# Performance work log

Hardware: AMD Instinct MI355X
Metric: run time of the kernel (lower is better)

## Reference

```python
import jax, jax.numpy as jnp
import numpy as np

GROUP_SIZES = [2048, 4096, 8192, 16384]
TOP_K = 64
L1_COEFF = 1e-3
AUX_PENALTY = 1e-2
N_BATCHES_TO_DEAD = 20
AUX_K_MULT = 16


def setup_inputs() -> dict:
    D = 1024
    S = sum(GROUP_SIZES)  # 30720
    B = 2048
    key = jax.random.key(0)
    k1, k2, k3 = jax.random.split(key, 3)
    x = jax.random.normal(k1, (B, D), dtype=jnp.float32)
    # kaiming_uniform-like init for W_enc [D, S]
    bound = np.sqrt(6.0 / D)
    W_enc = jax.random.uniform(k2, (D, S), jnp.float32, -bound, bound)
    # W_dec = W_enc.T row-normalized (as in __init__)
    W_dec = W_enc.T
    W_dec = W_dec / jnp.linalg.norm(W_dec, axis=-1, keepdims=True)
    b_dec = jnp.zeros((D,), jnp.float32)
    b_enc = jnp.zeros((S,), jnp.float32)
    num_batches_not_active = jax.random.randint(k3, (S,), 0, 40, dtype=jnp.int32)
    return dict(x=x, b_dec=b_dec, b_enc=b_enc, W_enc=W_enc, W_dec=W_dec,
                num_batches_not_active=num_batches_not_active)


def reference(x, b_dec, b_enc, W_enc, W_dec, num_batches_not_active):
    B, D = x.shape
    S = W_enc.shape[1]
    # encoder
    acts = jax.nn.relu((x - b_dec) @ W_enc + b_enc)  # [B, S]
    # global (batch-level) top-k over flattened activations + scatter back
    k = TOP_K * B
    flat = acts.reshape(-1)
    vals, idx = jax.lax.top_k(flat, k)
    acts_topk = jnp.zeros_like(flat).at[idx].set(vals).reshape(B, S)
    # hierarchical group-wise decode with per-group L2 losses
    bounds = np.concatenate([[0], np.cumsum(GROUP_SIZES)]).astype(int)
    recon = jnp.broadcast_to(b_dec, (B, D))
    l2_losses = []
    for i in range(len(GROUP_SIZES)):
        s, e = int(bounds[i]), int(bounds[i + 1])
        recon = recon + acts_topk[:, s:e] @ W_dec[s:e, :]
        l2_losses.append(jnp.mean((recon - x) ** 2))
    mean_l2_loss = jnp.mean(jnp.stack(l2_losses))
    l1_loss = L1_COEFF * jnp.mean(jnp.sum(jnp.abs(acts_topk), axis=-1))
    # auxiliary dead-feature loss
    dead = num_batches_not_active >= N_BATCHES_TO_DEAD  # [S] bool
    residual = jax.lax.stop_gradient(x - recon)
    k_aux = TOP_K * AUX_K_MULT * B  # assumes num_dead * B >= k_aux (holds here)
    masked = jnp.where(dead[None, :], acts, -jnp.inf)
    min_top_k_val = jax.lax.top_k(masked.reshape(-1), k_aux)[0][-1]
    min_top_k_val = jnp.where(jnp.isfinite(min_top_k_val), min_top_k_val, 0.0)
    acts_aux = jax.nn.relu(acts - min_top_k_val) * dead[None, :].astype(acts.dtype)
    recon_aux = acts_aux @ W_dec  # dead-only contribution (others zeroed)
    aux_loss = AUX_PENALTY * jnp.mean((recon_aux - residual) ** 2)
    aux_loss = jnp.where(jnp.any(dead), aux_loss, 0.0)
    total_loss = mean_l2_loss + l1_loss + aux_loss
    l0_norm = jnp.mean(jnp.sum((acts_topk > 0).astype(jnp.float32), axis=-1))
    return total_loss, mean_l2_loss, l1_loss, aux_loss, l0_norm, acts_topk, recon
```

## Files before the change

kernel.cpp:

```cpp
#include <hip/hip_runtime.h>

#define NB 2048
#define ND 1024
#define NS 30720
#define K_MAIN 131072LL
#define K_AUX  2097152LL
#define BAND_CAP 16384
#define SEL_CAP  8192
#define CANDA_CAP 65536
#define EPS_BAND 1e-3f
#define KSPLIT 4

#define OFF_SCAL 0
#define OFF_ACC  256
#define OFF_H1M  512
#define OFF_H1A  16896
#define OFF_H2M  33280
#define OFF_H2A  49664
#define OFF_ZERO_END 66048
#define OFF_DEAD 66048
#define OFF_SEL_IDX 98304
#define OFF_SEL_BITS 131072
#define OFF_BANDI 163840
#define OFF_BANDV 229376
#define OFF_CAB  360448
#define OFF_RAUX 1048576ULL
#define OFF_AH   (OFF_RAUX + (unsigned long long)KSPLIT * NB * ND * 4)
#define OFF_AL   (OFF_AH + 2048ULL*1024*2)
#define OFF_WHT  (OFF_AL + 2048ULL*1024*2)
#define OFF_WLT  (OFF_WHT + 30720ULL*1024*2)
#define WS_NEED_ENC (OFF_WLT + 30720ULL*1024*2)
#define OFF_AXB  OFF_AH
#define OFF_WDT  (OFF_AXB + 2048ULL*30720*2)
#define WS_NEED_AUX (OFF_WDT + 1024ULL*30720*2)

#define S_NDEAD 0
#define S_B1M 1
#define S_REM1M 2
#define S_B1A 3
#define S_REM1A 4
#define S_T24M 5
#define S_BLO 6
#define S_BHI 7
#define S_T24A 8
#define S_JA 9
#define S_NHI 10
#define S_BANDC 11
#define S_CCA 12
#define S_SELCNT 13
#define S_L0 14
#define S_MINBITS 15

#define A_L2_0 0
#define A_L1 4
#define A_AUX 5

typedef __attribute__((ext_vector_type(8))) short bf16x8;
typedef __attribute__((ext_vector_type(4))) float f32x4;

__device__ __forceinline__ float blk_reduce(float v, float* sred) {
    int t = threadIdx.x;
    #pragma unroll
    for (int o = 32; o > 0; o >>= 1) v += __shfl_down(v, o, 64);
    __syncthreads();
    if ((t & 63) == 0) sred[t >> 6] = v;
    __syncthreads();
    return sred[0] + sred[1] + sred[2] + sred[3];
}

__device__ __forceinline__ unsigned short f2bf(float f) {
    unsigned u = __float_as_uint(f);
    unsigned r = (u + 0x7FFFu + ((u >> 16) & 1u)) >> 16;
    return (unsigned short)r;
}
__device__ __forceinline__ float bf2f(unsigned short h) {
    return __uint_as_float(((unsigned)h) << 16);
}

#define GLD16(gp, lp) __builtin_amdgcn_global_load_lds( \
    (const __attribute__((address_space(1))) unsigned int*)(gp), \
    (__attribute__((address_space(3))) unsigned int*)(lp), 16, 0, 0)

__global__ void k_init(int* w) {
    int n = OFF_ZERO_END / 4;
    for (int i = blockIdx.x * blockDim.x + threadIdx.x; i < n; i += gridDim.x * blockDim.x)
        w[i] = 0;
}

__global__ void k_dead(const int* __restrict__ nbna, unsigned char* __restrict__ dead, int* scal) {
    int stride = gridDim.x * blockDim.x;
    int cnt = 0;
    for (int i = blockIdx.x * blockDim.x + threadIdx.x; i < NS; i += stride) {
        bool d = nbna[i] >= 20;
        dead[i] = d ? 1 : 0;
        cnt += d ? 1 : 0;
    }
    #pragma unroll
    for (int o = 32; o > 0; o >>= 1) cnt += __shfl_down(cnt, o, 64);
    if ((threadIdx.x & 63) == 0 && cnt) atomicAdd(&scal[S_NDEAD], cnt);
}

__global__ void k_prep_a(const float* __restrict__ x, const float* __restrict__ b_dec,
                         unsigned short* __restrict__ Ahg, unsigned short* __restrict__ Alg) {
    int stride = gridDim.x * blockDim.x;
    for (int i = blockIdx.x * blockDim.x + threadIdx.x; i < NB * ND; i += stride) {
        float v = x[i] - b_dec[i & (ND - 1)];
        unsigned short h = f2bf(v);
        unsigned short l = f2bf(v - bf2f(h));
        Ahg[i] = h; Alg[i] = l;
    }
}

__global__ __launch_bounds__(256) void k_prep_w(const float* __restrict__ W,
        unsigned short* __restrict__ WhT, unsigned short* __restrict__ WlT) {
    __shared__ float tile[32][33];
    int n0 = blockIdx.x * 32, k0 = blockIdx.y * 32;
    int t = threadIdx.x;
    int c = t & 31, r = t >> 5;
    #pragma unroll
    for (int it = 0; it < 4; it++)
        tile[r + it * 8][c] = W[(size_t)(k0 + r + it * 8) * NS + n0 + c];
    __syncthreads();
    int kl = t & 31, nl = t >> 5;
    #pragma unroll
    for (int it = 0; it < 4; it++) {
        float v = tile[kl][nl + it * 8];
        unsigned short h = f2bf(v);
        unsigned short l = f2bf(v - bf2f(h));
        size_t o = (size_t)(n0 + nl + it * 8) * ND + k0 + kl;
        WhT[o] = h; WlT[o] = l;
    }
}

#define ENC_STAGE(bufoff, p, gptr, r, ktn) GLD16((gptr) + (size_t)(r) * 128 * ND + (size_t)(ktn) * 32, \
    smem + (bufoff) + (p) * 8192 + (r) * 4096 + ldsw)

#define ENC_RD_AH(boff) { _Pragma("unroll") \
    for (int i = 0; i < 8; i++) ah[i] = *(const bf16x8*)&smem[(boff) + (arb + i * 16) * 32 + cph8]; }
#define ENC_RD_AL(boff) { _Pragma("unroll") \
    for (int i = 0; i < 8; i++) al[i] = *(const bf16x8*)&smem[(boff) + 8192 + (arb + i * 16) * 32 + cph8]; }
#define ENC_RD_BH(boff) { _Pragma("unroll") \
    for (int j = 0; j < 4; j++) bh[j] = *(const bf16x8*)&smem[(boff) + 2 * 8192 + (brb + j * 16) * 32 + cph8]; }
#define ENC_RD_BL(boff) { _Pragma("unroll") \
    for (int j = 0; j < 4; j++) bl[j] = *(const bf16x8*)&smem[(boff) + 3 * 8192 + (brb + j * 16) * 32 + cph8]; }

#define ENC_MFMA(AF, BF) { \
    asm volatile("s_waitcnt lgkmcnt(0)" ::: "memory"); \
    __builtin_amdgcn_sched_barrier(0); \
    __builtin_amdgcn_s_setprio(1); \
    _Pragma("unroll") for (int i = 0; i < 8; i++) \
        _Pragma("unroll") for (int j = 0; j < 4; j++) \
            acc[i][j] = __builtin_amdgcn_mfma_f32_16x16x32_bf16(AF[i], BF[j], acc[i][j], 0, 0, 0); \
    __builtin_amdgcn_s_setprio(0); }

__global__ __launch_bounds__(512, 2) void k_enc_mfma(
        const unsigned short* __restrict__ Ahg, const unsigned short* __restrict__ Alg,
        const unsigned short* __restrict__ WhT, const unsigned short* __restrict__ WlT,
        const float* __restrict__ b_enc, const unsigned char* __restrict__ dead,
        float* __restrict__ acts, int* __restrict__ h1m, int* __restrict__ h1a) {
    __shared__ unsigned short smem[65536];
    const int t = threadIdx.x;
    const int lane = t & 63, w = t >> 6;
    const int wm = w >> 2, wn = w & 3;
    const int flat = blockIdx.x;
    const int wg = (flat & 7) * 120 + (flat >> 3);
    const int n0 = (wg >> 3) * 256;
    const int m0 = (wg & 7) * 256;
    const int ln15 = lane & 15, q = lane >> 4;
    const int cph8 = ((q ^ ((lane >> 1) & 3)) << 3);

    const int srow = w * 16 + (lane >> 2);
    const int sq8 = (((lane & 3) ^ ((lane >> 3) & 3)) << 3);
    const unsigned short* gA  = Ahg + (size_t)(m0 + srow) * ND + sq8;
    const unsigned short* gAl = Alg + (size_t)(m0 + srow) * ND + sq8;
    const unsigned short* gB  = WhT + (size_t)(n0 + srow) * ND + sq8;
    const unsigned short* gBl = WlT + (size_t)(n0 + srow) * ND + sq8;
    const int ldsw = w * 512;

    f32x4 acc[8][4];
    #pragma unroll
    for (int i = 0; i < 8; i++)
        #pragma unroll
        for (int j = 0; j < 4; j++) acc[i][j] = (f32x4){0.f, 0.f, 0.f, 0.f};

    const int arb = wm * 128 + ln15;
    const int brb = wn * 64 + ln15;

    ENC_STAGE(0, 0, gA, 0, 0);  ENC_STAGE(0, 0, gA, 1, 0);
    ENC_STAGE(0, 2, gB, 0, 0);  ENC_STAGE(0, 2, gB, 1, 0);
    ENC_STAGE(0, 3, gBl, 0, 0); ENC_STAGE(0, 3, gBl, 1, 0);
    ENC_STAGE(0, 1, gAl, 0, 0); ENC_STAGE(0, 1, gAl, 1, 0);

    for (int kt = 0; kt < 31; ++kt) {
        const int cboff = (kt & 1) * 32768;
        const int nboff = cboff ^ 32768;
        const int kn = kt + 1;
        bf16x8 ah[8], bh[4], bl[4], al[8];

        ENC_STAGE(nboff, 0, gA, 0, kn);  ENC_STAGE(nboff, 0, gA, 1, kn);
        ENC_STAGE(nboff, 2, gB, 0, kn);  ENC_STAGE(nboff, 2, gB, 1, kn);
        asm volatile("s_waitcnt vmcnt(8)" ::: "memory");
        __builtin_amdgcn_s_barrier();
        ENC_RD_AH(cboff) ENC_RD_BH(cboff)
        ENC_MFMA(ah, bh)

        ENC_STAGE(nboff, 3, gBl, 0, kn); ENC_STAGE(nboff, 3, gBl, 1, kn);
        ENC_STAGE(nboff, 1, gAl, 0, kn); ENC_STAGE(nboff, 1, gAl, 1, kn);
        asm volatile("s_waitcnt vmcnt(8)" ::: "memory");
        __builtin_amdgcn_s_barrier();
        ENC_RD_BL(cboff)
        ENC_MFMA(ah, bl)

        ENC_RD_AL(cboff)
        ENC_MFMA(al, bh)
    }

    {
        const int cboff = 32768;
        bf16x8 ah[8], bh[4], bl[4], al[8];
        asm volatile("s_waitcnt vmcnt(4)" ::: "memory");
        __builtin_amdgcn_s_barrier();
        ENC_RD_AH(cboff) ENC_RD_BH(cboff)
        ENC_MFMA(ah, bh)
        asm volatile("s_waitcnt vmcnt(0)" ::: "memory");
        __builtin_amdgcn_s_barrier();
        ENC_RD_BL(cboff)
        ENC_MFMA(ah, bl)
        ENC_RD_AL(cboff)
        ENC_MFMA(al, bh)
    }

    __syncthreads();
    int* hm = (int*)smem;
    int* ha = hm + 4096;
    for (int i2 = t; i2 < 8192; i2 += 512) hm[i2] = 0;
    __syncthreads();

    int zc = 0, zca = 0;
    #pragma unroll
    for (int j = 0; j < 4; j++) {
        int n = n0 + wn * 64 + j * 16 + ln15;
        float be = b_enc[n];
        bool dd = dead[n] != 0;
        #pragma unroll
        for (int i = 0; i < 8; i++) {
            int mrow = m0 + wm * 128 + i * 16 + q * 4;
            #pragma unroll
            for (int rg = 0; rg < 4; rg++) {
                float v = fmaxf(acc[i][j][rg] + be, 0.f);
                acts[(size_t)(mrow + rg) * NS + n] = v;
                unsigned bits = __float_as_uint(v);
                if (bits == 0u) { zc++; zca += dd ? 1 : 0; }
                else {
                    atomicAdd(&hm[bits >> 20], 1);
                    if (dd) atomicAdd(&ha[bits >> 20], 1);
                }
            }
        }
    }
    #pragma unroll
    for (int o = 32; o > 0; o >>= 1) { zc += __shfl_down(zc, o, 64); zca += __shfl_down(zca, o, 64); }
    if ((t & 63) == 0) { if (zc) atomicAdd(&hm[0], zc); if (zca) atomicAdd(&ha[0], zca); }
    __syncthreads();
    for (int i2 = t; i2 < 4096; i2 += 512) {
        if (hm[i2]) atomicAdd(&h1m[i2], hm[i2]);
        if (ha[i2]) atomicAdd(&h1a[i2], ha[i2]);
    }
}

#define GBM 128
#define GBN 128
#define GBK 8
__global__ __launch_bounds__(256) void k_enc_gemm(const float* __restrict__ x,
        const float* __restrict__ b_dec, const float* __restrict__ b_enc,
        const float* __restrict__ W, float* __restrict__ acts) {
    __shared__ float As[GBK][GBM];
    __shared__ float Bs[GBK][GBN];
    const int t = threadIdx.x;
    const int tx = t & 15, ty = t >> 4;
    const int m0 = blockIdx.y * GBM, n0 = blockIdx.x * GBN;
    const int am = t >> 1, ak = (t & 1) * 4;
    const int bk = t >> 5, bnq = (t & 31) * 4;
    float acc[8][8];
    #pragma unroll
    for (int i = 0; i < 8; i++)
        #pragma unroll
        for (int j = 0; j < 8; j++) acc[i][j] = 0.f;
    for (int k0 = 0; k0 < ND; k0 += GBK) {
        float4 av = *(const float4*)(x + (size_t)(m0 + am) * ND + k0 + ak);
        float4 bd = *(const float4*)(b_dec + k0 + ak);
        As[ak + 0][am] = av.x - bd.x;
        As[ak + 1][am] = av.y - bd.y;
        As[ak + 2][am] = av.z - bd.z;
        As[ak + 3][am] = av.w - bd.w;
        *(float4*)&Bs[bk][bnq] = *(const float4*)(W + (size_t)(k0 + bk) * NS + n0 + bnq);
        __syncthreads();
        #pragma unroll
        for (int kk = 0; kk < GBK; kk++) {
            float a[8], b[8];
            *(float4*)&a[0] = *(const float4*)&As[kk][ty * 4];
            *(float4*)&a[4] = *(const float4*)&As[kk][64 + ty * 4];
            *(float4*)&b[0] = *(const float4*)&Bs[kk][tx * 4];
            *(float4*)&b[4] = *(const float4*)&Bs[kk][64 + tx * 4];
            #pragma unroll
            for (int i = 0; i < 8; i++)
                #pragma unroll
                for (int j = 0; j < 8; j++)
                    acc[i][j] = fmaf(a[i], b[j], acc[i][j]);
        }
        __syncthreads();
    }
    float be[8];
    #pragma unroll
    for (int j = 0; j < 4; j++) {
        be[j]     = b_enc[n0 + tx * 4 + j];
        be[4 + j] = b_enc[n0 + 64 + tx * 4 + j];
    }
    #pragma unroll
    for (int i = 0; i < 8; i++) {
        int row = m0 + ((i < 4) ? (ty * 4 + i) : (64 + ty * 4 + i - 4));
        float* orow = acts + (size_t)row * NS + n0;
        #pragma unroll
        for (int j = 0; j < 4; j++) {
            orow[tx * 4 + j]      = fmaxf(acc[i][j] + be[j], 0.f);
            orow[64 + tx * 4 + j] = fmaxf(acc[i][4 + j] + be[4 + j], 0.f);
        }
    }
}

__global__ __launch_bounds__(256) void k_hist1(const float* __restrict__ acts,
        const unsigned char* __restrict__ dead, int* h1m, int* h1a) {
    __shared__ int hm[4096], ha[4096];
    int t = threadIdx.x;
    for (int i = t; i < 4096; i += 256) { hm[i] = 0; ha[i] = 0; }
    __syncthreads();
    for (int row = blockIdx.x; row < NB; row += gridDim.x) {
        const float* pr = acts + (size_t)row * NS;
        for (int c = t; c < NS; c += 256) {
            unsigned bits = __float_as_uint(pr[c]);
            bool isz = (bits == 0u);
            bool dd = dead[c] != 0;
            unsigned long long mz = __ballot(isz);
            unsigned long long mza = __ballot(isz && dd);
            if ((t & 63) == 0) {
                int nz = __popcll(mz);
                if (nz) atomicAdd(&hm[0], nz);
                int nza = __popcll(mza);
                if (nza) atomicAdd(&ha[0], nza);
            }
            if (!isz) {
                atomicAdd(&hm[bits >> 20], 1);
                if (dd) atomicAdd(&ha[bits >> 20], 1);
            }
        }
    }
    __syncthreads();
    for (int i = t; i < 4096; i += 256) {
        if (hm[i]) atomicAdd(&h1m[i], hm[i]);
        if (ha[i]) atomicAdd(&h1a[i], ha[i]);
    }
}

__global__ void k_scan(const int* __restrict__ hist, int* scal, int mode) {
    __shared__ long long csum[256];
    __shared__ long long totsh;
    int t = threadIdx.x;
    int base = t * 16;
    int h[16];
    long long loc = 0;
    #pragma unroll
    for (int i = 0; i < 16; i++) { h[i] = hist[base + i]; loc += h[i]; }
    csum[t] = loc;
    __syncthreads();
    if (t == 0) {
        long long run = 0;
        for (int c = 255; c >= 0; c--) { long long tmp = csum[c]; csum[c] = run; run += tmp; }
        totsh = run;
    }
    __syncthreads();
    long long k;
    if (mode == 0) k = K_MAIN;
    else if (mode == 1) k = K_AUX;
    else if (mode == 2) k = (long long)scal[S_REM1M];
    else {
        if (scal[S_B1A] < 0) { if (t == 0) { scal[S_T24A] = -1; scal[S_MINBITS] = 0; } return; }
        k = (long long)scal[S_REM1A];
    }
    if (mode == 1 && k > totsh) { if (t == 0) scal[S_B1A] = -1; return; }
    long long cum = csum[t];
    int fb = -1; long long rem = 0;
    for (int i = 15; i >= 0; i--) {
        long long ca = cum;
        cum += h[i];
        if (ca < k && k <= cum) { fb = base + i; rem = k - ca; }
    }
    if (fb >= 0) {
        if (mode == 0)      { scal[S_B1M] = fb; scal[S_REM1M] = (int)rem; }
        else if (mode == 1) { scal[S_B1A] = fb; scal[S_REM1A] = (int)rem; }
        else if (mode == 2) {
            int t24 = (scal[S_B1M] << 12) | fb;
            scal[S_T24M] = t24;
            float center = __uint_as_float((((unsigned)t24) << 8) | 128u);
            float lo = center - EPS_BAND;
            if (lo < 0.f) lo = 0.f;
            scal[S_BLO] = (int)__float_as_uint(lo);
            scal[S_BHI] = (int)__float_as_uint(center + EPS_BAND);
        }
        else { scal[S_T24A] = (scal[S_B1A] << 12) | fb; scal[S_JA] = (int)rem; }
    }
}

__global__ __launch_bounds__(256) void k_hist2(const float* __restrict__ acts,
        const unsigned char* __restrict__ dead, const int* scal, int* h2m, int* h2a) {
    int b1m = scal[S_B1M], b1a = scal[S_B1A];
    int row = blockIdx.x, t = threadIdx.x;
    const float* pr = acts + (size_t)row * NS;
    for (int c = t; c < NS; c += 256) {
        unsigned bits = __float_as_uint(pr[c]);
        int hi = (int)(bits >> 20);
        if (hi == b1m) atomicAdd(&h2m[(bits >> 8) & 0xFFF], 1);
        if (b1a >= 0 && hi == b1a && dead[c]) atomicAdd(&h2a[(bits >> 8) & 0xFFF], 1);
    }
}

__global__ __launch_bounds__(256) void k_collect(const float* __restrict__ acts,
        const unsigned char* __restrict__ dead, int* scal,
        int* bandi, unsigned* cab) {
    int row = blockIdx.x, t = threadIdx.x;
    unsigned blo = (unsigned)scal[S_BLO], bhi = (unsigned)scal[S_BHI];
    int t24a = scal[S_T24A];
    const float* pr = acts + (size_t)row * NS;
    int cnt = 0;
    for (int c = t; c < NS; c += 256) {
        unsigned bits = __float_as_uint(pr[c]);
        if (bits > bhi) cnt++;
        else if (bits >= blo) {
            int p = atomicAdd(&scal[S_BANDC], 1);
            if (p < BAND_CAP) bandi[p] = row * NS + c;
        }
        if (t24a >= 0 && (bits >> 8) == (unsigned)t24a && dead[c]) {
            int p = atomicAdd(&scal[S_CCA], 1);
            if (p < CANDA_CAP) cab[p] = bits;
        }
    }
    #pragma unroll
    for (int o = 32; o > 0; o >>= 1) cnt += __shfl_down(cnt, o, 64);
    __shared__ int s2[4];
    if ((t & 63) == 0) s2[t >> 6] = cnt;
    __syncthreads();
    if (t == 0) {
        int tot = s2[0] + s2[1] + s2[2] + s2[3];
        if (tot) atomicAdd(&scal[S_NHI], tot);
    }
}

__global__ __launch_bounds__(256) void k_resolve(const unsigned* __restrict__ cab, int* scal) {
    __shared__ int h[256];
    int t = threadIdx.x;
    h[t] = 0;
    __syncthreads();
    int t24a = scal[S_T24A];
    if (t24a < 0) { if (t == 0) scal[S_MINBITS] = 0; return; }
    int cnt = min(scal[S_CCA], CANDA_CAP);
    int ja = scal[S_JA];
    for (int e = t; e < cnt; e += 256) atomicAdd(&h[cab[e] & 0xFF], 1);
    __syncthreads();
    if (t == 0) {
        long long cum = 0; int L = 0;
        for (int b = 255; b >= 0; b--) {
            long long ca = cum; cum += h[b];
            if (ca < ja && ja <= cum) { L = b; break; }
        }
        scal[S_MINBITS] = (int)((((unsigned)t24a) << 8) | (unsigned)L);
    }
}

__global__ __launch_bounds__(256) void k_band_re(const float* __restrict__ x,
        const float* __restrict__ b_dec, const float* __restrict__ b_enc,
        const float* __restrict__ W, const int* scal,
        const int* __restrict__ bandi, double* __restrict__ bandv) {
    int n = min(scal[S_BANDC], BAND_CAP);
    int t = threadIdx.x;
    __shared__ double sd[4];
    for (int e = blockIdx.x; e < n; e += gridDim.x) {
        int idx = bandi[e];
        int r = idx / NS, c = idx - r * NS;
        double s = 0.0;
        #pragma unroll
        for (int j = 0; j < 4; j++) {
            int d = t + j * 256;
            s += ((double)x[(size_t)r * ND + d] - (double)b_dec[d]) * (double)W[(size_t)d * NS + c];
        }
        #pragma unroll
        for (int o = 32; o > 0; o >>= 1) s += __shfl_down(s, o, 64);
        if ((t & 63) == 0) sd[t >> 6] = s;
        __syncthreads();
        if (t == 0) {
            double v = sd[0] + sd[1] + sd[2] + sd[3] + (double)b_enc[c];
            bandv[e] = fmax(v, 0.0);
        }
        __syncthreads();
    }
}

__global__ __launch_bounds__(256) void k_band_sel(int* scal,
        const int* __restrict__ bandi, const double* __restrict__ bandv,
        int* sel_idx, unsigned* sel_bits) {
    int n = min(scal[S_BANDC], BAND_CAP);
    int need = (int)(K_MAIN - (long long)scal[S_NHI]);
    if (need < 0) need = 0;
    if (need > n) need = n;
    int t = threadIdx.x;
    for (int e = t; e < n; e += 256) {
        double v = bandv[e];
        int idx = bandi[e];
        int rank = 0;
        for (int j = 0; j < n; j++) {
            double vj = bandv[j];
            rank += (vj > v || (vj == v && bandi[j] < idx)) ? 1 : 0;
        }
        if (rank < need) {
            int p = atomicAdd(&scal[S_SELCNT], 1);
            if (p < SEL_CAP) { sel_idx[p] = idx; sel_bits[p] = __float_as_uint((float)v); }
        }
    }
}

__global__ __launch_bounds__(256) void k_decode(float* __restrict__ acts,
        const float* __restrict__ x, const float* __restrict__ b_dec, const float* __restrict__ Wd,
        float* __restrict__ recon, const unsigned char* __restrict__ dead,
        const int* __restrict__ sel_idx, unsigned short* __restrict__ axb,
        int* scal, double* acc, int fuse) {
    int row = blockIdx.x, t = threadIdx.x;
    unsigned blo = (unsigned)scal[S_BLO], bhi = (unsigned)scal[S_BHI];
    float minval = __uint_as_float((unsigned)scal[S_MINBITS]);
    int selcnt = min(scal[S_SELCNT], SEL_CAP);
    __shared__ int lj[2048];
    __shared__ float lv[2048];
    __shared__ int lcnt;
    __shared__ float sred[4];
    const int d0 = t * 4;
    float4 r;
    r.x = b_dec[d0]; r.y = b_dec[d0 + 1]; r.z = b_dec[d0 + 2]; r.w = b_dec[d0 + 3];
    float4 xv = *(const float4*)(x + (size_t)row * ND + d0);
    float* arow = acts + (size_t)row * NS;
    unsigned short* xrow = axb + (size_t)row * NS;
    float l1 = 0.f; int kcnt = 0;
    const int bnds[5] = {0, 2048, 6144, 14336, NS};
    for (int g = 0; g < 4; g++) {
        for (int c0 = bnds[g]; c0 < bnds[g + 1]; c0 += 2048) {
            __syncthreads();
            if (t == 0) lcnt = 0;
            __syncthreads();
            #pragma unroll
            for (int u = 0; u < 8; u++) {
                int c = c0 + u * 256 + t;
                float v = arow[c];
                unsigned bits = __float_as_uint(v);
                bool strict = bits > bhi;
                bool keep = strict;
                if (!keep && bits >= blo) {
                    int flat = row * NS + c;
                    for (int e = 0; e < selcnt; e++)
                        if (sel_idx[e] == flat) { keep = true; break; }
                }
                if (keep) { int p = atomicAdd(&lcnt, 1); lj[p] = c; lv[p] = v; }
                if (fuse) {
                    if (strict) { l1 += v; kcnt++; }
                    arow[c] = strict ? v : 0.f;
                    float o = (dead[c] && v > minval) ? (v - minval) : 0.f;
                    xrow[c] = f2bf(o);
                }
            }
            __syncthreads();
            int n = lcnt;
            for (int e = 0; e < n; e++) {
                float a_ = lv[e];
                float4 w = *(const float4*)(Wd + (size_t)lj[e] * ND + d0);
                r.x = fmaf(a_, w.x, r.x);
                r.y = fmaf(a_, w.y, r.y);
                r.z = fmaf(a_, w.z, r.z);
                r.w = fmaf(a_, w.w, r.w);
            }
        }
        float dx = r.x - xv.x, dy = r.y - xv.y, dz = r.z - xv.z, dw = r.w - xv.w;
        float ss = dx * dx + dy * dy + dz * dz + dw * dw;
        float tot = blk_reduce(ss, sred);
        if (t == 0) atomicAdd(&acc[A_L2_0 + g], (double)tot);
    }
    float* orow = recon + (size_t)row * ND + d0;
    orow[0] = r.x; orow[1] = r.y; orow[2] = r.z; orow[3] = r.w;
    if (fuse) {
        #pragma unroll
        for (int o = 32; o > 0; o >>= 1) { l1 += __shfl_down(l1, o, 64); kcnt += __shfl_down(kcnt, o, 64); }
        __shared__ float s1[4];
        __shared__ int s2[4];
        if ((t & 63) == 0) { s1[t >> 6] = l1; s2[t >> 6] = kcnt; }
        __syncthreads();
        if (t == 0) {
            atomicAdd(&acc[A_L1], (double)(s1[0] + s1[1] + s1[2] + s1[3]));
            atomicAdd(&scal[S_L0], s2[0] + s2[1] + s2[2] + s2[3]);
        }
    }
}

__global__ __launch_bounds__(256) void k_aux_pack(const float* __restrict__ acts,
        const unsigned char* __restrict__ dead, const int* scal,
        unsigned short* __restrict__ axb) {
    int row = blockIdx.x, t = threadIdx.x;
    float minval = __uint_as_float((unsigned)scal[S_MINBITS]);
    const float* arow = acts + (size_t)row * NS;
    unsigned short* orow = axb + (size_t)row * NS;
    for (int c = t; c < NS; c += 256) {
        float v = arow[c];
        float o = (dead[c] && v > minval) ? (v - minval) : 0.f;
        orow[c] = f2bf(o);
    }
}

__global__ __launch_bounds__(256) void k_prep_wd(const float* __restrict__ Wd,
        unsigned short* __restrict__ WdT) {
    __shared__ float tile[32][33];
    int s0 = blockIdx.x * 32, d0 = blockIdx.y * 32;
    int t = threadIdx.x;
    int c = t & 31, r = t >> 5;
    #pragma unroll
    for (int it = 0; it < 4; it++)
        tile[r + it * 8][c] = Wd[(size_t)(s0 + r + it * 8) * ND + d0 + c];
    __syncthreads();
    int sl = t & 31, dl = t >> 5;
    #pragma unroll
    for (int it = 0; it < 4; it++)
        WdT[(size_t)(d0 + dl + it * 8) * NS + s0 + sl] = f2bf(tile[sl][dl + it * 8]);
}

__global__ __launch_bounds__(256) void k_aux_mfma(
        const unsigned short* __restrict__ axb, const unsigned short* __restrict__ WdT,
        float* __restrict__ raux) {
    __shared__ unsigned short As[128 * 32], Bs[128 * 32];
    const int t = threadIdx.x;
    const int lane = t & 63, w = t >> 6;
    const int wm = w >> 1, wn = w & 1;
    const int m0 = blockIdx.y * 128, n0 = blockIdx.x * 128;
    const int kbase = blockIdx.z * (NS / KSPLIT);
    const int ln15 = lane & 15, q = lane >> 4;

    f32x4 acc[4][4];
    #pragma unroll
    for (int i = 0; i < 4; i++)
        #pragma unroll
        for (int j = 0; j < 4; j++) acc[i][j] = (f32x4){0.f, 0.f, 0.f, 0.f};

    const unsigned short* gbase;
    unsigned short* lbase;
    if (w < 2) { gbase = axb + (size_t)(m0 + w * 64) * NS; lbase = As + w * 64 * 32; }
    else       { gbase = WdT + (size_t)(n0 + (w - 2) * 64) * NS; lbase = Bs + (w - 2) * 64 * 32; }
    const unsigned short* glane = gbase + (size_t)(lane >> 2) * NS + (lane & 3) * 8 + kbase;

    for (int k0 = 0; k0 < NS / KSPLIT; k0 += 32) {
        __syncthreads();
        #pragma unroll
        for (int ch = 0; ch < 4; ch++)
            GLD16(glane + (size_t)ch * 16 * NS + k0, lbase + ch * 512);
        __syncthreads();

        bf16x8 af[4];
        #pragma unroll
        for (int i = 0; i < 4; i++)
            af[i] = *(const bf16x8*)&As[(wm * 64 + i * 16 + ln15) * 32 + q * 8];
        #pragma unroll
        for (int j = 0; j < 4; j++) {
            bf16x8 bf = *(const bf16x8*)&Bs[(wn * 64 + j * 16 + ln15) * 32 + q * 8];
            #pragma unroll
            for (int i = 0; i < 4; i++)
                acc[i][j] = __builtin_amdgcn_mfma_f32_16x16x32_bf16(af[i], bf, acc[i][j], 0, 0, 0);
        }
    }
    float* rz = raux + (size_t)blockIdx.z * NB * ND;
    #pragma unroll
    for (int j = 0; j < 4; j++) {
        int n = n0 + wn * 64 + j * 16 + ln15;
        #pragma unroll
        for (int i = 0; i < 4; i++) {
            int mrow = m0 + wm * 64 + i * 16 + q * 4;
            #pragma unroll
            for (int rg = 0; rg < 4; rg++)
                rz[(size_t)(mrow + rg) * ND + n] = acc[i][j][rg];
        }
    }
}

__global__ __launch_bounds__(256) void k_aux_diff(const float* __restrict__ raux,
        const float* __restrict__ x, const float* __restrict__ recon, double* acc) {
    __shared__ float sred[4];
    float ss = 0.f;
    int stride = gridDim.x * blockDim.x;
    for (int i = blockIdx.x * blockDim.x + threadIdx.x; i < NB * ND; i += stride) {
        float ra = raux[i];
        #pragma unroll
        for (int z = 1; z < KSPLIT; z++) ra += raux[(size_t)z * NB * ND + i];
        float d = ra - (x[i] - recon[i]);
        ss += d * d;
    }
    float tot = blk_reduce(ss, sred);
    if (threadIdx.x == 0) atomicAdd(&acc[A_AUX], (double)tot);
}

__global__ __launch_bounds__(256) void k_aux(const float* __restrict__ acts,
        const unsigned char* __restrict__ dead, const float* __restrict__ x,
        const float* __restrict__ recon, const float* __restrict__ Wd,
        const int* scal, double* acc) {
    int row = blockIdx.x, t = threadIdx.x;
    float minval = __uint_as_float((unsigned)scal[S_MINBITS]);
    __shared__ int lj[2048];
    __shared__ float lv[2048];
    __shared__ int lcnt;
    __shared__ float sred[4];
    float4 r = {0.f, 0.f, 0.f, 0.f};
    const float* arow = acts + (size_t)row * NS;
    const int d0 = t * 4;
    for (int c0 = 0; c0 < NS; c0 += 2048) {
        __syncthreads();
        if (t == 0) lcnt = 0;
        __syncthreads();
        #pragma unroll
        for (int u = 0; u < 8; u++) {
            int c = c0 + u * 256 + t;
            float v = arow[c];
            if (dead[c] && v > minval) {
                int p = atomicAdd(&lcnt, 1);
                lj[p] = c; lv[p] = v - minval;
            }
        }
        __syncthreads();
        int n = lcnt;
        for (int e = 0; e < n; e++) {
            float a_ = lv[e];
            float4 w = *(const float4*)(Wd + (size_t)lj[e] * ND + d0);
            r.x = fmaf(a_, w.x, r.x);
            r.y = fmaf(a_, w.y, r.y);
            r.z = fmaf(a_, w.z, r.z);
            r.w = fmaf(a_, w.w, r.w);
        }
    }
    const float* xr = x + (size_t)row * ND + d0;
    const float* rr = recon + (size_t)row * ND + d0;
    float dx = r.x - (xr[0] - rr[0]);
    float dy = r.y - (xr[1] - rr[1]);
    float dz = r.z - (xr[2] - rr[2]);
    float dw = r.w - (xr[3] - rr[3]);
    float ss = dx * dx + dy * dy + dz * dz + dw * dw;
    float tot = blk_reduce(ss, sred);
    if (t == 0) atomicAdd(&acc[A_AUX], (double)tot);
}

__global__ __launch_bounds__(256) void k_topk_write(float* __restrict__ out, const int* scal, double* acc, int* scalw) {
    unsigned bhi = (unsigned)scal[S_BHI];
    float l1 = 0.f;
    int cnt = 0;
    const long long vstart = 8, nvec = 15728639;
    long long stride = (long long)gridDim.x * blockDim.x;
    for (long long i = (long long)blockIdx.x * blockDim.x + threadIdx.x; i < nvec; i += stride) {
        float4* p = (float4*)(out + vstart) + i;
        float4 v = *p;
        #define PROC(F) { unsigned b = __float_as_uint(v.F); if (b > bhi) { l1 += v.F; cnt++; } else v.F = 0.f; }
        PROC(x) PROC(y) PROC(z) PROC(w)
        #undef PROC
        *p = v;
    }
    if (blockIdx.x == 0 && threadIdx.x == 0) {
        const long long head[4] = {5, 6, 7, 62914564LL};
        for (int q = 0; q < 4; q++) {
            float v = out[head[q]];
            unsigned b = __float_as_uint(v);
            if (b > bhi) { l1 += v; cnt++; } else out[head[q]] = 0.f;
        }
    }
    int t = threadIdx.x;
    #pragma unroll
    for (int o = 32; o > 0; o >>= 1) { l1 += __shfl_down(l1, o, 64); cnt += __shfl_down(cnt, o, 64); }
    __shared__ float s1[4];
    __shared__ int s2[4];
    if ((t & 63) == 0) { s1[t >> 6] = l1; s2[t >> 6] = cnt; }
    __syncthreads();
    if (t == 0) {
        atomicAdd(&acc[A_L1], (double)(s1[0] + s1[1] + s1[2] + s1[3]));
        atomicAdd(&scalw[S_L0], s2[0] + s2[1] + s2[2] + s2[3]);
    }
}

__global__ __launch_bounds__(256) void k_selwrite(float* __restrict__ acts, const int* __restrict__ sel_idx,
        const unsigned* __restrict__ sel_bits, int* scal, double* acc) {
    int t = threadIdx.x;
    int n = min(scal[S_SELCNT], SEL_CAP);
    float l1 = 0.f;
    for (int e = t; e < n; e += 256) {
        float v = __uint_as_float(sel_bits[e]);
        acts[sel_idx[e]] = v;
        l1 += v;
    }
    #pragma unroll
    for (int o = 32; o > 0; o >>= 1) l1 += __shfl_down(l1, o, 64);
    __shared__ float s1[4];
    if ((t & 63) == 0) s1[t >> 6] = l1;
    __syncthreads();
    if (t == 0) {
        atomicAdd(&acc[A_L1], (double)(s1[0] + s1[1] + s1[2] + s1[3]));
        atomicAdd(&scal[S_L0], n);
    }
}

__global__ void k_final(float* out, const int* scal, const double* acc) {
    if (threadIdx.x == 0 && blockIdx.x == 0) {
        double ml2 = (acc[0] + acc[1] + acc[2] + acc[3]) * 0.25 / ((double)NB * ND);
        double l1 = 1e-3 * acc[A_L1] / (double)NB;
        double aux = (scal[S_NDEAD] > 0) ? (1e-2 * acc[A_AUX] / ((double)NB * ND)) : 0.0;
        out[0] = (float)(ml2 + l1 + aux);
        out[1] = (float)ml2;
        out[2] = (float)l1;
        out[3] = (float)aux;
        out[4] = (float)scal[S_L0] / (float)NB;
    }
}

extern "C" void kernel_launch(void* const* d_in, const int* in_sizes, int n_in,
                              void* d_out, int out_size, void* d_ws, size_t ws_size,
                              hipStream_t stream) {
    const float* x     = (const float*)d_in[0];
    const float* b_dec = (const float*)d_in[1];
    const float* b_enc = (const float*)d_in[2];
    const float* W_enc = (const float*)d_in[3];
    const float* W_dec = (const float*)d_in[4];
    const int*   nbna  = (const int*)d_in[5];

    float* out = (float*)d_out;
    float* acts  = out + 5;
    float* recon = out + 5 + (size_t)NB * NS;

    char* ws = (char*)d_ws;
    int*    scal = (int*)(ws + OFF_SCAL);
    double* acc  = (double*)(ws + OFF_ACC);
    int*    h1m  = (int*)(ws + OFF_H1M);
    int*    h1a  = (int*)(ws + OFF_H1A);
    int*    h2m  = (int*)(ws + OFF_H2M);
    int*    h2a  = (int*)(ws + OFF_H2A);
    unsigned char* dead = (unsigned char*)(ws + OFF_DEAD);
    int*      sel_idx  = (int*)(ws + OFF_SEL_IDX);
    unsigned* sel_bits = (unsigned*)(ws + OFF_SEL_BITS);
    int*      bandi = (int*)(ws + OFF_BANDI);
    double*   bandv = (double*)(ws + OFF_BANDV);
    unsigned* cab   = (unsigned*)(ws + OFF_CAB);
    float*    raux  = (float*)(ws + OFF_RAUX);
    unsigned short* Ahg = (unsigned short*)(ws + OFF_AH);
    unsigned short* Alg = (unsigned short*)(ws + OFF_AL);
    unsigned short* WhT = (unsigned short*)(ws + OFF_WHT);
    unsigned short* WlT = (unsigned short*)(ws + OFF_WLT);
    unsigned short* axb = (unsigned short*)(ws + OFF_AXB);
    unsigned short* WdT = (unsigned short*)(ws + OFF_WDT);

    const bool use_mfma     = (ws_size >= WS_NEED_ENC);
    const bool use_aux_gemm = (ws_size >= WS_NEED_AUX);

    k_init<<<64, 256, 0, stream>>>((int*)d_ws);
    k_dead<<<60, 256, 0, stream>>>(nbna, dead, scal);
    if (use_mfma) {
        k_prep_a<<<512, 256, 0, stream>>>(x, b_dec, Ahg, Alg);
        k_prep_w<<<dim3(NS / 32, ND / 32), 256, 0, stream>>>(W_enc, WhT, WlT);
        k_enc_mfma<<<(NB / 256) * (NS / 256), 512, 0, stream>>>(Ahg, Alg, WhT, WlT, b_enc, dead, acts, h1m, h1a);
    } else {
        k_enc_gemm<<<dim3(NS / GBN, NB / GBM), 256, 0, stream>>>(x, b_dec, b_enc, W_enc, acts);
        k_hist1<<<1024, 256, 0, stream>>>(acts, dead, h1m, h1a);
    }
    k_scan<<<1, 256, 0, stream>>>(h1m, scal, 0);
    k_scan<<<1, 256, 0, stream>>>(h1a, scal, 1);
    k_hist2<<<NB, 256, 0, stream>>>(acts, dead, scal, h2m, h2a);
    k_scan<<<1, 256, 0, stream>>>(h2m, scal, 2);
    k_scan<<<1, 256, 0, stream>>>(h2a, scal, 3);
    k_collect<<<NB, 256, 0, stream>>>(acts, dead, scal, bandi, cab);
    k_resolve<<<1, 256, 0, stream>>>(cab, scal);
    k_band_re<<<512, 256, 0, stream>>>(x, b_dec, b_enc, W_enc, scal, bandi, bandv);
    k_band_sel<<<1, 256, 0, stream>>>(scal, bandi, bandv, sel_idx, sel_bits);
    if (use_aux_gemm) {
        k_decode<<<NB, 256, 0, stream>>>(acts, x, b_dec, W_dec, recon, dead, sel_idx, axb, scal, acc, 1);
        k_prep_wd<<<dim3(NS / 32, ND / 32), 256, 0, stream>>>(W_dec, WdT);
        k_aux_mfma<<<dim3(ND / 128, NB / 128, KSPLIT), 256, 0, stream>>>(axb, WdT, raux);
        k_aux_diff<<<512, 256, 0, stream>>>(raux, x, recon, acc);
    } else {
        k_decode<<<NB, 256, 0, stream>>>(acts, x, b_dec, W_dec, recon, dead, sel_idx, axb, scal, acc, 0);
        k_aux<<<NB, 256, 0, stream>>>(acts, dead, x, recon, W_dec, scal, acc);
        k_topk_write<<<4096, 256, 0, stream>>>(out, scal, acc, scal);
    }
    k_selwrite<<<1, 256, 0, stream>>>(acts, sel_idx, sel_bits, scal, acc);
    k_final<<<1, 64, 0, stream>>>(out, scal, acc);
}
```

Before: 1.901 ms.

## Double-buffer aux MFMA GEMM with swizzled LDS and pack encoder histograms

```diff
diff --git a/kernel.cpp b/kernel.cpp
--- a/kernel.cpp
+++ b/kernel.cpp
@@ -231,17 +231,17 @@
     }
 
     __syncthreads();
-    int* hm = (int*)smem;
-    int* ha = hm + 4096;
-    for (int i2 = t; i2 < 8192; i2 += 512) hm[i2] = 0;
-    __syncthreads();
-
+    int* hh = (int*)smem;
+    for (int i2 = t; i2 < 16384; i2 += 512) hh[i2] = 0;
+    __syncthreads();
+
+    const int ln3 = lane & 3;
     int zc = 0, zca = 0;
     #pragma unroll
     for (int j = 0; j < 4; j++) {
         int n = n0 + wn * 64 + j * 16 + ln15;
         float be = b_enc[n];
-        bool dd = dead[n] != 0;
+        int dd = dead[n] ? 1 : 0;
         #pragma unroll
         for (int i = 0; i < 8; i++) {
             int mrow = m0 + wm * 128 + i * 16 + q * 4;
@@ -250,21 +250,22 @@
                 float v = fmaxf(acc[i][j][rg] + be, 0.f);
                 acts[(size_t)(mrow + rg) * NS + n] = v;
                 unsigned bits = __float_as_uint(v);
-                if (bits == 0u) { zc++; zca += dd ? 1 : 0; }
-                else {
-                    atomicAdd(&hm[bits >> 20], 1);
-                    if (dd) atomicAdd(&ha[bits >> 20], 1);
-                }
+                if (bits == 0u) { zc++; zca += dd; }
+                else atomicAdd(&hh[((bits >> 20) << 2) | ln3], 1 + (dd << 16));
             }
         }
     }
     #pragma unroll
     for (int o = 32; o > 0; o >>= 1) { zc += __shfl_down(zc, o, 64); zca += __shfl_down(zca, o, 64); }
-    if ((t & 63) == 0) { if (zc) atomicAdd(&hm[0], zc); if (zca) atomicAdd(&ha[0], zca); }
-    __syncthreads();
-    for (int i2 = t; i2 < 4096; i2 += 512) {
-        if (hm[i2]) atomicAdd(&h1m[i2], hm[i2]);
-        if (ha[i2]) atomicAdd(&h1a[i2], ha[i2]);
+    if ((t & 63) == 0 && (zc | zca)) atomicAdd(&hh[w & 3], zc + (zca << 16));
+    __syncthreads();
+    for (int b2 = t; b2 < 4096; b2 += 512) {
+        unsigned w0 = (unsigned)hh[b2 * 4 + 0], w1 = (unsigned)hh[b2 * 4 + 1];
+        unsigned w2 = (unsigned)hh[b2 * 4 + 2], w3 = (unsigned)hh[b2 * 4 + 3];
+        int m = (int)((w0 & 0xFFFFu) + (w1 & 0xFFFFu) + (w2 & 0xFFFFu) + (w3 & 0xFFFFu));
+        int a = (int)((w0 >> 16) + (w1 >> 16) + (w2 >> 16) + (w3 >> 16));
+        if (m) atomicAdd(&h1m[b2], m);
+        if (a) atomicAdd(&h1a[b2], a);
     }
 }
 
@@ -637,13 +638,15 @@
 __global__ __launch_bounds__(256) void k_aux_mfma(
         const unsigned short* __restrict__ axb, const unsigned short* __restrict__ WdT,
         float* __restrict__ raux) {
-    __shared__ unsigned short As[128 * 32], Bs[128 * 32];
+    __shared__ unsigned short smem[16384];
     const int t = threadIdx.x;
     const int lane = t & 63, w = t >> 6;
     const int wm = w >> 1, wn = w & 1;
     const int m0 = blockIdx.y * 128, n0 = blockIdx.x * 128;
     const int kbase = blockIdx.z * (NS / KSPLIT);
     const int ln15 = lane & 15, q = lane >> 4;
+    const int cph8 = ((q ^ ((lane >> 1) & 3)) << 3);
+    const int sq8 = (((lane & 3) ^ ((lane >> 3) & 3)) << 3);
 
     f32x4 acc[4][4];
     #pragma unroll
@@ -652,29 +655,44 @@
         for (int j = 0; j < 4; j++) acc[i][j] = (f32x4){0.f, 0.f, 0.f, 0.f};
 
     const unsigned short* gbase;
-    unsigned short* lbase;
-    if (w < 2) { gbase = axb + (size_t)(m0 + w * 64) * NS; lbase = As + w * 64 * 32; }
-    else       { gbase = WdT + (size_t)(n0 + (w - 2) * 64) * NS; lbase = Bs + (w - 2) * 64 * 32; }
-    const unsigned short* glane = gbase + (size_t)(lane >> 2) * NS + (lane & 3) * 8 + kbase;
-
-    for (int k0 = 0; k0 < NS / KSPLIT; k0 += 32) {
-        __syncthreads();
-        #pragma unroll
-        for (int ch = 0; ch < 4; ch++)
-            GLD16(glane + (size_t)ch * 16 * NS + k0, lbase + ch * 512);
-        __syncthreads();
-
-        bf16x8 af[4];
+    int ldst;
+    if (w < 2) { gbase = axb + (size_t)(m0 + w * 64) * NS; ldst = w * 64 * 32; }
+    else       { gbase = WdT + (size_t)(n0 + (w - 2) * 64) * NS; ldst = 4096 + (w - 2) * 64 * 32; }
+    const unsigned short* glane = gbase + (size_t)(lane >> 2) * NS + sq8 + kbase;
+    ldst += (lane >> 2) * 32 + (lane & 3) * 8;
+
+    #pragma unroll
+    for (int ch = 0; ch < 4; ch++)
+        GLD16(glane + (size_t)ch * 16 * NS, smem + ldst + ch * 512);
+
+    const int NKT = (NS / KSPLIT) / 32;
+    for (int kt = 0; kt < NKT; ++kt) {
+        const int cb = (kt & 1) * 8192;
+        const int nb = cb ^ 8192;
+        asm volatile("s_waitcnt vmcnt(0)" ::: "memory");
+        __builtin_amdgcn_s_barrier();
+        __builtin_amdgcn_sched_barrier(0);
+        if (kt < NKT - 1) {
+            #pragma unroll
+            for (int ch = 0; ch < 4; ch++)
+                GLD16(glane + (size_t)ch * 16 * NS + (size_t)(kt + 1) * 32, smem + nb + ldst + ch * 512);
+        }
+        bf16x8 af[4], bf[4];
         #pragma unroll
         for (int i = 0; i < 4; i++)
-            af[i] = *(const bf16x8*)&As[(wm * 64 + i * 16 + ln15) * 32 + q * 8];
-        #pragma unroll
-        for (int j = 0; j < 4; j++) {
-            bf16x8 bf = *(const bf16x8*)&Bs[(wn * 64 + j * 16 + ln15) * 32 + q * 8];
+            af[i] = *(const bf16x8*)&smem[cb + (wm * 64 + i * 16 + ln15) * 32 + cph8];
+        #pragma unroll
+        for (int j = 0; j < 4; j++)
+            bf[j] = *(const bf16x8*)&smem[cb + 4096 + (wn * 64 + j * 16 + ln15) * 32 + cph8];
+        asm volatile("s_waitcnt lgkmcnt(0)" ::: "memory");
+        __builtin_amdgcn_sched_barrier(0);
+        __builtin_amdgcn_s_setprio(1);
+        #pragma unroll
+        for (int j = 0; j < 4; j++)
             #pragma unroll
             for (int i = 0; i < 4; i++)
-                acc[i][j] = __builtin_amdgcn_mfma_f32_16x16x32_bf16(af[i], bf, acc[i][j], 0, 0, 0);
-        }
+                acc[i][j] = __builtin_amdgcn_mfma_f32_16x16x32_bf16(af[i], bf[j], acc[i][j], 0, 0, 0);
+        __builtin_amdgcn_s_setprio(0);
     }
     float* rz = raux + (size_t)blockIdx.z * NB * ND;
     #pragma unroll
```

After: 1.884 ms. About the same (-0.9%).
